# Optimization experiments

Hardware: AMD Instinct MI355X
Metric: run time of the kernel (lower is better)

## Reference

```python
import jax, jax.numpy as jnp
import numpy as np

N = 50000   # total nodes across batched graphs
E = 800000  # total edges
F = 30      # input node features
G = 256     # number of graphs in the disjoint batch
CH = [128, 64, 32]
N_LABELS = 2


def setup_inputs() -> dict:
    key = jax.random.key(0)
    ks = jax.random.split(key, 16)
    x = jax.random.normal(ks[0], (N, F), dtype=jnp.float32)
    edge_weight = jax.random.uniform(ks[1], (E,), dtype=jnp.float32)
    edge_row = jax.random.randint(ks[2], (E,), 0, N, dtype=jnp.int32)
    edge_col = jax.random.randint(ks[3], (E,), 0, N, dtype=jnp.int32)
    seg = jnp.sort(jax.random.randint(ks[4], (N,), 0, G, dtype=jnp.int32))
    # GCSConv params: out = A @ (x W1) + x W2 + b, per layer
    dims = [F] + CH
    params = {}
    kk = 5
    for l in range(3):
        fin, fout = dims[l], dims[l + 1]
        s = 1.0 / np.sqrt(fin)
        params[f"w1_{l+1}"] = jax.random.uniform(ks[kk], (fin, fout), minval=-s, maxval=s, dtype=jnp.float32); kk += 1
        params[f"w2_{l+1}"] = jax.random.uniform(ks[kk], (fin, fout), minval=-s, maxval=s, dtype=jnp.float32); kk += 1
        params[f"b_{l+1}"] = jnp.zeros((fout,), dtype=jnp.float32)
    sd = 1.0 / np.sqrt(CH[-1])
    params["wd"] = jax.random.uniform(ks[kk], (CH[-1], N_LABELS), minval=-sd, maxval=sd, dtype=jnp.float32)
    params["bd"] = jnp.zeros((N_LABELS,), dtype=jnp.float32)
    return {"x": x, "edge_weight": edge_weight, "edge_row": edge_row,
            "edge_col": edge_col, "seg": seg, **params}


def _gcs_conv(x, ew, er, ec, w1, w2, b):
    # spektral GCSConv: relu(A @ (x W1) + x W2 + b) with sparse A in COO form
    h = x @ w1                                   # [N, Fout]
    msgs = ew[:, None] * h[ec]                   # gather along edges [E, Fout]
    agg = jax.ops.segment_sum(msgs, er, num_segments=N)  # SpMM scatter [N, Fout]
    return jax.nn.relu(agg + x @ w2 + b)


def reference(x, edge_weight, edge_row, edge_col, seg,
              w1_1, w2_1, b_1, w1_2, w2_2, b_2, w1_3, w2_3, b_3, wd, bd):
    h = _gcs_conv(x, edge_weight, edge_row, edge_col, w1_1, w2_1, b_1)
    h = _gcs_conv(h, edge_weight, edge_row, edge_col, w1_2, w2_2, b_2)
    h = _gcs_conv(h, edge_weight, edge_row, edge_col, w1_3, w2_3, b_3)
    # GlobalAvgPool: segment mean over graph ids
    sums = jax.ops.segment_sum(h, seg, num_segments=G)               # [G, 32]
    cnts = jax.ops.segment_sum(jnp.ones((N,), h.dtype), seg, num_segments=G)
    pooled = sums / jnp.maximum(cnts, 1.0)[:, None]
    return jax.nn.softmax(pooled @ wd + bd, axis=-1)                 # [G, 2]
```

## Files before the change

### kernel.cpp

```cpp
#include <hip/hip_runtime.h>
#include <hip/hip_fp16.h>

#define N_NODES 50000
#define N_EDGES 800000
#define N_GRAPHS 256
#define NCB 196
#define CHUNK 3125
#define MBLK 782

typedef _Float16 f16x8 __attribute__((ext_vector_type(8)));
typedef float    f32x4 __attribute__((ext_vector_type(4)));

__global__ __launch_bounds__(256)
void hist_prep(const int* __restrict__ ER, const float* __restrict__ X,
               const int* __restrict__ SEG,
               const float* __restrict__ W1, const float* __restrict__ W2,
               const float* __restrict__ W12, const float* __restrict__ W22,
               const float* __restrict__ W13, const float* __restrict__ W23,
               int* __restrict__ ghist, __half* __restrict__ XPh,
               int* __restrict__ start,
               __half* __restrict__ W1f, __half* __restrict__ W2f,
               __half* __restrict__ W3f, float* __restrict__ PS)
{
    int b = blockIdx.x;
    int t = threadIdx.x;
    if (b < 256) {
        __shared__ int h[NCB];
        for (int i = t; i < NCB; i += 256) h[i] = 0;
        __syncthreads();
        int lo = b * CHUNK, hi = lo + CHUNK;
        for (int e = lo + t; e < hi; e += 256) atomicAdd(&h[ER[e] >> 8], 1);
        __syncthreads();
        for (int i = t; i < NCB; i += 256) ghist[i * 256 + b] = h[i];
        return;
    }
    int bid = b - 256;
    if (bid < 6250) {
        int idx = bid * 256 + t;
        int n = idx >> 5;
        int c = idx & 31;
        float v = (c < 30) ? X[n * 30 + c] : 0.f;
        XPh[(size_t)n * 32 + c] = __float2half(v);
    } else if (bid < 6446) {
        int n = (bid - 6250) * 256 + t;
        if (n >= N_NODES) return;
        int g = SEG[n];
        int gprev = (n == 0) ? -1 : SEG[n - 1];
        for (int gg = gprev + 1; gg <= g; ++gg) start[gg] = n;
        if (n == N_NODES - 1)
            for (int gg = g + 1; gg <= N_GRAPHS; ++gg) start[gg] = N_NODES;
    } else if (bid < 6558) {
        int idx = (bid - 6446) * 256 + t;
        if (idx < 8192) {
            int i = idx & 7, c = (idx >> 3) & 15, g = (idx >> 7) & 3;
            int s = (idx >> 9) & 1, n = idx >> 10;
            int k = s * 32 + g * 8 + i, col = n * 16 + c;
            float w = 0.f;
            if (k < 30) w = W1[k * 128 + col];
            else if (k >= 32 && k < 62) w = W2[(k - 32) * 128 + col];
            W1f[idx] = __float2half(w);
        } else if (idx < 24576) {
            int o = idx - 8192;
            int i = o & 7, c = (o >> 3) & 15, g = (o >> 7) & 3;
            int s = (o >> 9) & 3, n = o >> 11;
            int k = s * 32 + g * 8 + i, col = n * 16 + c;
            float w = (col < 64) ? W12[k * 64 + col] : W22[k * 64 + col - 64];
            W2f[o] = __float2half(w);
        } else {
            int o = idx - 24576;
            int i = o & 7, c = (o >> 3) & 15, g = (o >> 7) & 3;
            int s = (o >> 9) & 1, n = o >> 10;
            int k = s * 32 + g * 8 + i, col = n * 16 + c;
            float w = (col < 32) ? W13[k * 32 + col] : W23[k * 32 + col - 32];
            W3f[o] = __float2half(w);
        }
    } else {
        int idx = (bid - 6558) * 256 + t;
        PS[idx] = 0.f;
    }
}

__global__ __launch_bounds__(256)
void scan1(int* __restrict__ ghist, int* __restrict__ bsum)
{
    __shared__ int s[256];
    int t = threadIdx.x, b = blockIdx.x;
    int i = b * 256 + t;
    int v = ghist[i];
    s[t] = v;
    __syncthreads();
    for (int off = 1; off < 256; off <<= 1) {
        int u = (t >= off) ? s[t - off] : 0;
        __syncthreads();
        s[t] += u;
        __syncthreads();
    }
    ghist[i] = s[t] - v;
    if (t == 255) bsum[b] = s[255];
}

__global__ __launch_bounds__(256)
void c_scatter(const int* __restrict__ ER, const int* __restrict__ EC,
               const float* __restrict__ EW, const int* __restrict__ ghist,
               const int* __restrict__ bsum, unsigned int* __restrict__ tmp_sd,
               __half* __restrict__ tmp_w)
{
    __shared__ int s[256];
    __shared__ int cur[NCB];
    int t = threadIdx.x, blk = blockIdx.x;
    int v = (t < NCB) ? bsum[t] : 0;
    s[t] = v;
    __syncthreads();
    for (int off = 1; off < 256; off <<= 1) {
        int u = (t >= off) ? s[t - off] : 0;
        __syncthreads();
        s[t] += u;
        __syncthreads();
    }
    if (t < NCB) cur[t] = (s[t] - v) + ghist[t * 256 + blk];
    __syncthreads();
    int lo = blk * CHUNK, hi = lo + CHUNK;
    for (int e = lo + t; e < hi; e += 256) {
        int d = ER[e];
        int pos = atomicAdd(&cur[d >> 8], 1);
        tmp_sd[pos] = (unsigned int)EC[e] | ((unsigned int)(d & 255) << 16);
        tmp_w[pos] = __float2half(EW[e]);
    }
}

__device__ __forceinline__ void fma8h(float4& a0, float4& a1, float w,
                                      const uint4& raw)
{
    const __half2* hp = (const __half2*)&raw;
    float2 f0 = __half22float2(hp[0]);
    float2 f1 = __half22float2(hp[1]);
    float2 f2 = __half22float2(hp[2]);
    float2 f3 = __half22float2(hp[3]);
    a0.x = fmaf(w, f0.x, a0.x); a0.y = fmaf(w, f0.y, a0.y);
    a0.z = fmaf(w, f1.x, a0.z); a0.w = fmaf(w, f1.y, a0.w);
    a1.x = fmaf(w, f2.x, a1.x); a1.y = fmaf(w, f2.y, a1.y);
    a1.z = fmaf(w, f3.x, a1.z); a1.w = fmaf(w, f3.y, a1.w);
}

__device__ __forceinline__ unsigned int relu2(unsigned int u)
{
    unsigned int lo = (u & 0x8000u)     ? 0u : (u & 0x0000FFFFu);
    unsigned int hi = (u & 0x80000000u) ? 0u : (u & 0xFFFF0000u);
    return lo | hi;
}

__global__ __launch_bounds__(512)
void bsort_aggx(const unsigned int* __restrict__ tmp_sd, const __half* __restrict__ tmp_w,
                const int* __restrict__ bsum, const __half* __restrict__ XPh,
                unsigned int* __restrict__ packed, int* __restrict__ rowptr,
                __half* __restrict__ CIa)
{
    __shared__ int s[256];
    __shared__ int hist[256];
    __shared__ int cur[256];
    __shared__ int r0arr[257];
    int t = threadIdx.x, b = blockIdx.x;

    if (t < 256) s[t] = (t < NCB) ? bsum[t] : 0;
    __syncthreads();
    for (int off = 1; off < 256; off <<= 1) {
        int u = 0;
        if (t < 256 && t >= off) u = s[t - off];
        __syncthreads();
        if (t < 256) s[t] += u;
        __syncthreads();
    }
    int cntb = bsum[b];
    int base = s[b] - cntb;
    int end  = base + cntb;
    __syncthreads();

    if (t < 256) hist[t] = 0;
    __syncthreads();
    for (int j = base + t; j < end; j += 512)
        atomicAdd(&hist[(tmp_sd[j] >> 16) & 255], 1);
    __syncthreads();
    int hv = 0;
    if (t < 256) { hv = hist[t]; s[t] = hv; }
    __syncthreads();
    for (int off = 1; off < 256; off <<= 1) {
        int u = 0;
        if (t < 256 && t >= off) u = s[t - off];
        __syncthreads();
        if (t < 256) s[t] += u;
        __syncthreads();
    }
    if (t < 256) {
        int excl = s[t] - hv;
        int n = b * 256 + t;
        if (n < N_NODES) rowptr[n] = base + excl;
        if (b == NCB - 1 && t == 0) rowptr[N_NODES] = N_EDGES;
        r0arr[t] = base + excl;
        cur[t] = base + excl;
        if (t == 0) r0arr[256] = end;
    }
    __syncthreads();
    for (int j = base + t; j < end; j += 512) {
        unsigned int sd = tmp_sd[j];
        unsigned short hb = __half_as_ushort(tmp_w[j]);
        int pos = atomicAdd(&cur[(sd >> 16) & 255], 1);
        packed[pos] = (sd & 0xFFFF) | ((unsigned int)hb << 16);
    }
    __syncthreads();

    #pragma unroll
    for (int pass = 0; pass < 2; ++pass) {
        int local = pass * 128 + (t >> 2);
        int q = t & 3;
        int n = b * 256 + local;
        if (n < N_NODES) {
            int r0 = r0arr[local], r1 = r0arr[local + 1];
            float4 acc0 = make_float4(0.f, 0.f, 0.f, 0.f);
            float4 acc1 = make_float4(0.f, 0.f, 0.f, 0.f);
            int j = r0;
            for (; j + 3 < r1; j += 4) {
                unsigned int ra = packed[j],     rb = packed[j + 1];
                unsigned int rc = packed[j + 2], rd = packed[j + 3];
                uint4 rawa = *(const uint4*)(XPh + (size_t)(ra & 0xFFFF) * 32 + q * 8);
                uint4 rawb = *(const uint4*)(XPh + (size_t)(rb & 0xFFFF) * 32 + q * 8);
                uint4 rawc = *(const uint4*)(XPh + (size_t)(rc & 0xFFFF) * 32 + q * 8);
                uint4 rawd = *(const uint4*)(XPh + (size_t)(rd & 0xFFFF) * 32 + q * 8);
                float wa = __half2float(__ushort_as_half((unsigned short)(ra >> 16)));
                float wb = __half2float(__ushort_as_half((unsigned short)(rb >> 16)));
                float wc = __half2float(__ushort_as_half((unsigned short)(rc >> 16)));
                float wd = __half2float(__ushort_as_half((unsigned short)(rd >> 16)));
                fma8h(acc0, acc1, wa, rawa);
                fma8h(acc0, acc1, wb, rawb);
                fma8h(acc0, acc1, wc, rawc);
                fma8h(acc0, acc1, wd, rawd);
            }
            for (; j < r1; ++j) {
                unsigned int r = packed[j];
                uint4 raw = *(const uint4*)(XPh + (size_t)(r & 0xFFFF) * 32 + q * 8);
                float w = __half2float(__ushort_as_half((unsigned short)(r >> 16)));
                fma8h(acc0, acc1, w, raw);
            }
            __half2 hb2[4];
            hb2[0] = __float22half2_rn(make_float2(acc0.x, acc0.y));
            hb2[1] = __float22half2_rn(make_float2(acc0.z, acc0.w));
            hb2[2] = __float22half2_rn(make_float2(acc1.x, acc1.y));
            hb2[3] = __float22half2_rn(make_float2(acc1.z, acc1.w));
            *(uint4*)(CIa + (size_t)n * 32 + q * 8) = *(uint4*)&hb2[0];
        }
    }
}

__global__ __launch_bounds__(256)
void dense12_mfma(const __half* __restrict__ CIa, const __half* __restrict__ XPh,
                  const __half* __restrict__ W1f, const float* __restrict__ B1,
                  const __half* __restrict__ W2f, const float* __restrict__ B2,
                  __half* __restrict__ H2a, __half* __restrict__ H2b,
                  __half* __restrict__ A2a, __half* __restrict__ A2b)
{
    __shared__ __align__(16) __half As[64 * 72];
    __shared__ __align__(16) __half Hs[64 * 136];
    const int tid = threadIdx.x;
    const int m0 = blockIdx.x * 64;
    const int lane = tid & 63;
    const int w  = tid >> 6;
    const int lr = lane & 15;
    const int lg = lane >> 4;

    for (int idx = tid; idx < 512; idx += 256) {
        int row = idx >> 3, c8 = idx & 7;
        int gm = m0 + row;
        uint4 v = make_uint4(0, 0, 0, 0);
        if (gm < N_NODES) {
            const __half* src = (c8 < 4) ? (CIa + (size_t)gm * 32 + c8 * 8)
                                         : (XPh + (size_t)gm * 32 + (c8 - 4) * 8);
            v = *(const uint4*)src;
        }
        *(uint4*)(As + row * 72 + c8 * 8) = v;
    }
    __syncthreads();

    f32x4 acc[4][2];
    #pragma unroll
    for (int m = 0; m < 4; ++m)
        #pragma unroll
        for (int j = 0; j < 2; ++j)
            acc[m][j] = (f32x4){0.f, 0.f, 0.f, 0.f};

    #pragma unroll
    for (int s = 0; s < 2; ++s) {
        f16x8 a[4];
        #pragma unroll
        for (int m = 0; m < 4; ++m)
            a[m] = *(const f16x8*)(As + (m * 16 + lr) * 72 + s * 32 + lg * 8);
        #pragma unroll
        for (int j = 0; j < 2; ++j) {
            const int n = 2 * w + j;
            f16x8 b = *(const f16x8*)(W1f + (((n * 2 + s) * 4 + lg) * 16 + lr) * 8);
            #pragma unroll
            for (int m = 0; m < 4; ++m)
                acc[m][j] = __builtin_amdgcn_mfma_f32_16x16x32_f16(a[m], b, acc[m][j], 0, 0, 0);
        }
    }

    #pragma unroll
    for (int j = 0; j < 2; ++j) {
        const int n = 2 * w + j;
        const float bias = B1[n * 16 + lr];
        #pragma unroll
        for (int m = 0; m < 4; ++m)
            #pragma unroll
            for (int r = 0; r < 4; ++r) {
                float v = fmaxf(acc[m][j][r] + bias, 0.f);
                Hs[(m * 16 + lg * 4 + r) * 136 + n * 16 + lr] = __float2half(v);
            }
    }
    __syncthreads();

    f32x4 acc2[4][2];
    #pragma unroll
    for (int m = 0; m < 4; ++m)
        #pragma unroll
        for (int j = 0; j < 2; ++j)
            acc2[m][j] = (f32x4){0.f, 0.f, 0.f, 0.f};

    #pragma unroll
    for (int s = 0; s < 4; ++s) {
        f16x8 a[4];
        #pragma unroll
        for (int m = 0; m < 4; ++m)
            a[m] = *(const f16x8*)(Hs + (m * 16 + lr) * 136 + s * 32 + lg * 8);
        #pragma unroll
        for (int j = 0; j < 2; ++j) {
            const int n = 2 * w + j;
            f16x8 b = *(const f16x8*)(W2f + (((n * 4 + s) * 4 + lg) * 16 + lr) * 8);
            #pragma unroll
            for (int m = 0; m < 4; ++m)
                acc2[m][j] = __builtin_amdgcn_mfma_f32_16x16x32_f16(a[m], b, acc2[m][j], 0, 0, 0);
        }
    }
    __syncthreads();

    #pragma unroll
    for (int j = 0; j < 2; ++j) {
        const int n = 2 * w + j;
        const float bias = (n >= 4) ? B2[(n - 4) * 16 + lr] : 0.f;
        #pragma unroll
        for (int m = 0; m < 4; ++m)
            #pragma unroll
            for (int r = 0; r < 4; ++r)
                Hs[(m * 16 + lg * 4 + r) * 136 + n * 16 + lr] =
                    __float2half(acc2[m][j][r] + bias);
    }
    __syncthreads();

    for (int idx = tid; idx < 1024; idx += 256) {
        int row = idx >> 4, c8 = idx & 15;
        int gm = m0 + row;
        if (gm < N_NODES) {
            uint4 v = *(const uint4*)(Hs + row * 136 + c8 * 8);
            __half* dst;
            switch (c8 >> 2) {
            case 0:  dst = H2a; break;
            case 1:  dst = H2b; break;
            case 2:  dst = A2a; break;
            default: dst = A2b; break;
            }
            *(uint4*)(dst + (size_t)gm * 32 + (c8 & 3) * 8) = v;
        }
    }
}

__global__ __launch_bounds__(256)
void dense3_mfma(const __half* __restrict__ A2a, const __half* __restrict__ A2b,
                 const __half* __restrict__ W3f,
                 const float* __restrict__ B3, __half* __restrict__ H3h,
                 __half* __restrict__ B2h)
{
    __shared__ __align__(16) __half As[64 * 72];
    __shared__ __align__(16) __half Os[64 * 72];
    const int tid = threadIdx.x;
    const int m0 = blockIdx.x * 64;
    const int lane = tid & 63;
    const int w  = tid >> 6;
    const int lr = lane & 15;
    const int lg = lane >> 4;

    for (int idx = tid; idx < 512; idx += 256) {
        int row = idx >> 3, c8 = idx & 7;
        int gm = m0 + row;
        uint4 v = make_uint4(0, 0, 0, 0);
        if (gm < N_NODES) {
            const __half* src = (c8 < 4) ? (A2a + (size_t)gm * 32 + c8 * 8)
                                         : (A2b + (size_t)gm * 32 + (c8 - 4) * 8);
            v = *(const uint4*)src;
        }
        v.x = relu2(v.x); v.y = relu2(v.y); v.z = relu2(v.z); v.w = relu2(v.w);
        *(uint4*)(As + row * 72 + c8 * 8) = v;
    }
    __syncthreads();

    f32x4 acc[4];
    #pragma unroll
    for (int m = 0; m < 4; ++m) acc[m] = (f32x4){0.f, 0.f, 0.f, 0.f};

    #pragma unroll
    for (int s = 0; s < 2; ++s) {
        f16x8 b = *(const f16x8*)(W3f + (((w * 2 + s) * 4 + lg) * 16 + lr) * 8);
        #pragma unroll
        for (int m = 0; m < 4; ++m) {
            f16x8 a = *(const f16x8*)(As + (m * 16 + lr) * 72 + s * 32 + lg * 8);
            acc[m] = __builtin_amdgcn_mfma_f32_16x16x32_f16(a, b, acc[m], 0, 0, 0);
        }
    }

    const float bias = (w >= 2) ? B3[(w - 2) * 16 + lr] : 0.f;
    #pragma unroll
    for (int m = 0; m < 4; ++m)
        #pragma unroll
        for (int r = 0; r < 4; ++r)
            Os[(m * 16 + lg * 4 + r) * 72 + w * 16 + lr] =
                __float2half(acc[m][r] + bias);
    __syncthreads();

    for (int idx = tid; idx < 512; idx += 256) {
        int row = idx >> 3, c8 = idx & 7;
        int gm = m0 + row;
        if (gm < N_NODES) {
            uint4 v = *(const uint4*)(Os + row * 72 + c8 * 8);
            if (c8 < 4) *(uint4*)(H3h + (size_t)gm * 32 + c8 * 8) = v;
            else        *(uint4*)(B2h + (size_t)gm * 32 + (c8 - 4) * 8) = v;
        }
    }
}

template<int FOUT>
__global__ __launch_bounds__(256)
void spmm_h(const __half* __restrict__ H, const int* __restrict__ rowptr,
            const unsigned int* __restrict__ packed, __half* __restrict__ AGGh)
{
    constexpr int T = FOUT / 8;
    int tid = threadIdx.x;
    int local = tid / T;
    int q = tid % T;
    int n = blockIdx.x * (256 / T) + local;
    if (n >= N_NODES) return;
    int r0 = rowptr[n], r1 = rowptr[n + 1];
    __half* ap = AGGh + (size_t)n * FOUT + q * 8;
    float4 acc0, acc1;
    {
        uint4 raw = *(const uint4*)ap;
        const __half2* hp = (const __half2*)&raw;
        float2 f0 = __half22float2(hp[0]);
        float2 f1 = __half22float2(hp[1]);
        float2 f2 = __half22float2(hp[2]);
        float2 f3 = __half22float2(hp[3]);
        acc0 = make_float4(f0.x, f0.y, f1.x, f1.y);
        acc1 = make_float4(f2.x, f2.y, f3.x, f3.y);
    }
    int j = r0;
    for (; j + 3 < r1; j += 4) {
        unsigned int ra = packed[j],     rb = packed[j + 1];
        unsigned int rc = packed[j + 2], rd = packed[j + 3];
        uint4 rawa = *(const uint4*)(H + (size_t)(ra & 0xFFFF) * FOUT + q * 8);
        uint4 rawb = *(const uint4*)(H + (size_t)(rb & 0xFFFF) * FOUT + q * 8);
        uint4 rawc = *(const uint4*)(H + (size_t)(rc & 0xFFFF) * FOUT + q * 8);
        uint4 rawd = *(const uint4*)(H + (size_t)(rd & 0xFFFF) * FOUT + q * 8);
        float wa = __half2float(__ushort_as_half((unsigned short)(ra >> 16)));
        float wb = __half2float(__ushort_as_half((unsigned short)(rb >> 16)));
        float wc = __half2float(__ushort_as_half((unsigned short)(rc >> 16)));
        float wd = __half2float(__ushort_as_half((unsigned short)(rd >> 16)));
        fma8h(acc0, acc1, wa, rawa);
        fma8h(acc0, acc1, wb, rawb);
        fma8h(acc0, acc1, wc, rawc);
        fma8h(acc0, acc1, wd, rawd);
    }
    for (; j < r1; ++j) {
        unsigned int r = packed[j];
        uint4 raw = *(const uint4*)(H + (size_t)(r & 0xFFFF) * FOUT + q * 8);
        float w = __half2float(__ushort_as_half((unsigned short)(r >> 16)));
        fma8h(acc0, acc1, w, raw);
    }
    __half2 hb[4];
    hb[0] = __float22half2_rn(make_float2(acc0.x, acc0.y));
    hb[1] = __float22half2_rn(make_float2(acc0.z, acc0.w));
    hb[2] = __float22half2_rn(make_float2(acc1.x, acc1.y));
    hb[3] = __float22half2_rn(make_float2(acc1.z, acc1.w));
    *(uint4*)ap = *(uint4*)&hb[0];
}

__global__ __launch_bounds__(256)
void spmm_pool(const __half* __restrict__ H, const int* __restrict__ rowptr,
               const unsigned int* __restrict__ packed,
               const __half* __restrict__ Bse, const int* __restrict__ SEG,
               float* __restrict__ PS)
{
    __shared__ float ps[65][32];
    int tid = threadIdx.x;
    int local = tid >> 2;
    int q = tid & 3;
    int n0 = blockIdx.x * 64;
    int n = n0 + local;
    for (int i = tid; i < 65 * 32; i += 256) ((float*)ps)[i] = 0.f;
    __syncthreads();
    int g0 = SEG[n0];
    if (n < N_NODES) {
        int g = SEG[n];
        int r0 = rowptr[n], r1 = rowptr[n + 1];
        float4 acc0, acc1;
        {
            uint4 raw = *(const uint4*)(Bse + (size_t)n * 32 + q * 8);
            const __half2* hp = (const __half2*)&raw;
            float2 f0 = __half22float2(hp[0]);
            float2 f1 = __half22float2(hp[1]);
            float2 f2 = __half22float2(hp[2]);
            float2 f3 = __half22float2(hp[3]);
            acc0 = make_float4(f0.x, f0.y, f1.x, f1.y);
            acc1 = make_float4(f2.x, f2.y, f3.x, f3.y);
        }
        int j = r0;
        for (; j + 3 < r1; j += 4) {
            unsigned int ra = packed[j],     rb = packed[j + 1];
            unsigned int rc = packed[j + 2], rd = packed[j + 3];
            uint4 rawa = *(const uint4*)(H + (size_t)(ra & 0xFFFF) * 32 + q * 8);
            uint4 rawb = *(const uint4*)(H + (size_t)(rb & 0xFFFF) * 32 + q * 8);
            uint4 rawc = *(const uint4*)(H + (size_t)(rc & 0xFFFF) * 32 + q * 8);
            uint4 rawd = *(const uint4*)(H + (size_t)(rd & 0xFFFF) * 32 + q * 8);
            float wa = __half2float(__ushort_as_half((unsigned short)(ra >> 16)));
            float wb = __half2float(__ushort_as_half((unsigned short)(rb >> 16)));
            float wc = __half2float(__ushort_as_half((unsigned short)(rc >> 16)));
            float wd = __half2float(__ushort_as_half((unsigned short)(rd >> 16)));
            fma8h(acc0, acc1, wa, rawa);
            fma8h(acc0, acc1, wb, rawb);
            fma8h(acc0, acc1, wc, rawc);
            fma8h(acc0, acc1, wd, rawd);
        }
        for (; j < r1; ++j) {
            unsigned int r = packed[j];
            uint4 raw = *(const uint4*)(H + (size_t)(r & 0xFFFF) * 32 + q * 8);
            float w = __half2float(__ushort_as_half((unsigned short)(r >> 16)));
            fma8h(acc0, acc1, w, raw);
        }
        float* dst = &ps[g - g0][q * 8];
        atomicAdd(&dst[0], fmaxf(acc0.x, 0.f));
        atomicAdd(&dst[1], fmaxf(acc0.y, 0.f));
        atomicAdd(&dst[2], fmaxf(acc0.z, 0.f));
        atomicAdd(&dst[3], fmaxf(acc0.w, 0.f));
        atomicAdd(&dst[4], fmaxf(acc1.x, 0.f));
        atomicAdd(&dst[5], fmaxf(acc1.y, 0.f));
        atomicAdd(&dst[6], fmaxf(acc1.z, 0.f));
        atomicAdd(&dst[7], fmaxf(acc1.w, 0.f));
    }
    __syncthreads();
    int nlast = n0 + 63;
    if (nlast >= N_NODES) nlast = N_NODES - 1;
    int span = SEG[nlast] - g0 + 1;
    for (int i = tid; i < span * 32; i += 256) {
        float v = ps[i >> 5][i & 31];
        if (v != 0.f)
            atomicAdd(&PS[(size_t)(g0 + (i >> 5)) * 32 + (i & 31)], v);
    }
}

__global__ __launch_bounds__(256)
void head_kernel(const float* __restrict__ PS, const int* __restrict__ start,
                 const float* __restrict__ WD, const float* __restrict__ BD,
                 float* __restrict__ OUT)
{
    int g = threadIdx.x;
    int s = start[g], e = start[g + 1];
    float inv = (e > s) ? 1.0f / (float)(e - s) : 1.0f;
    float l0 = 0.f, l1 = 0.f;
    #pragma unroll
    for (int j = 0; j < 32; ++j) {
        float p = PS[g * 32 + j] * inv;
        l0 = fmaf(p, WD[j * 2 + 0], l0);
        l1 = fmaf(p, WD[j * 2 + 1], l1);
    }
    l0 += BD[0]; l1 += BD[1];
    float m = fmaxf(l0, l1);
    float e0 = expf(l0 - m), e1 = expf(l1 - m);
    float si = 1.0f / (e0 + e1);
    OUT[g * 2 + 0] = e0 * si;
    OUT[g * 2 + 1] = e1 * si;
}

extern "C" void kernel_launch(void* const* d_in, const int* in_sizes, int n_in,
                              void* d_out, int out_size, void* d_ws, size_t ws_size,
                              hipStream_t stream)
{
    const float* x    = (const float*)d_in[0];
    const float* ew   = (const float*)d_in[1];
    const int*   er   = (const int*)d_in[2];
    const int*   ec   = (const int*)d_in[3];
    const int*   seg  = (const int*)d_in[4];
    const float* w1_1 = (const float*)d_in[5];
    const float* w2_1 = (const float*)d_in[6];
    const float* b_1  = (const float*)d_in[7];
    const float* w1_2 = (const float*)d_in[8];
    const float* w2_2 = (const float*)d_in[9];
    const float* b_2  = (const float*)d_in[10];
    const float* w1_3 = (const float*)d_in[11];
    const float* w2_3 = (const float*)d_in[12];
    const float* b_3  = (const float*)d_in[13];
    const float* wd   = (const float*)d_in[14];
    const float* bd   = (const float*)d_in[15];

    float* ws = (float*)d_ws;
    int*   IW = (int*)d_ws;
    __half* XPh    = (__half*)ws;
    __half* CIa    = (__half*)(ws + 800000);
    unsigned int* tmp_sd = (unsigned int*)(ws + 1600000);
    __half* tmp_w  = (__half*)(ws + 2400000);
    __half* H2a    = (__half*)(ws + 3200000);
    __half* H2b    = (__half*)(ws + 4000000);
    __half* A2a    = (__half*)(ws + 4800000);
    __half* A2b    = (__half*)(ws + 5600000);
    __half* H3h    = (__half*)(ws + 6400000);
    __half* B2h    = (__half*)(ws + 7200000);
    unsigned int* packed = (unsigned int*)(IW + 8000000);
    int*    rowptr = IW + 9000000;
    int*    ghist  = IW + 9060000;
    int*    bsum   = IW + 9115000;
    int*    start  = IW + 9120000;
    __half* W1f    = (__half*)(ws + 9125000);
    __half* W2f    = (__half*)(ws + 9130000);
    __half* W3f    = (__half*)(ws + 9139000);
    float*  PS     = ws + 9145000;

    dim3 blk(256);

    hist_prep<<<dim3(256 + 6590), blk, 0, stream>>>(er, x, seg, w1_1, w2_1,
                                                    w1_2, w2_2, w1_3, w2_3,
                                                    ghist, XPh, start,
                                                    W1f, W2f, W3f, PS);
    scan1<<<dim3(NCB), blk, 0, stream>>>(ghist, bsum);
    c_scatter<<<dim3(256), blk, 0, stream>>>(er, ec, ew, ghist, bsum, tmp_sd, tmp_w);
    bsort_aggx<<<dim3(NCB), dim3(512), 0, stream>>>(tmp_sd, tmp_w, bsum, XPh,
                                                    packed, rowptr, CIa);

    dense12_mfma<<<dim3(MBLK), blk, 0, stream>>>(CIa, XPh, W1f, b_1,
                                                 W2f, b_2, H2a, H2b, A2a, A2b);
    spmm_h<32><<<dim3(MBLK), blk, 0, stream>>>(H2a, rowptr, packed, A2a);
    spmm_h<32><<<dim3(MBLK), blk, 0, stream>>>(H2b, rowptr, packed, A2b);
    dense3_mfma<<<dim3(MBLK), blk, 0, stream>>>(A2a, A2b, w1_3 ? W3f : W3f, b_3, H3h, B2h);
    spmm_pool<<<dim3(MBLK), blk, 0, stream>>>(H3h, rowptr, packed, B2h, seg, PS);
    head_kernel<<<dim3(1), blk, 0, stream>>>(PS, start, wd, bd, (float*)d_out);
}
```

Baseline: 190.5 us.

## Fuse layer-2 SpMM into layer-3 dense MFMA kernel with 64-wide rows

Merges the two 32-column spmm_h passes and dense3_mfma into one kernel, spmm_dense3. It gathers 64-wide half rows of H2, adds the self term, applies ReLU and writes straight into shared memory, where the MFMA product for layer 3 reads it. H2 and A2 are now stored as contiguous 64-column rows, so each edge gather is a single 128-byte row read instead of two separate 64-byte passes. This removes two kernel launches and the global-memory round trip of the layer-2 aggregate. In exchange it uses 512-thread blocks, and the irregular gather now sits in the same kernel as the MFMA phase.

```diff
diff --git a/kernel.cpp b/kernel.cpp
--- a/kernel.cpp
+++ b/kernel.cpp
@@ -142,13 +142,6 @@
     a1.z = fmaf(w, f3.x, a1.z); a1.w = fmaf(w, f3.y, a1.w);
 }
 
-__device__ __forceinline__ unsigned int relu2(unsigned int u)
-{
-    unsigned int lo = (u & 0x8000u)     ? 0u : (u & 0x0000FFFFu);
-    unsigned int hi = (u & 0x80000000u) ? 0u : (u & 0xFFFF0000u);
-    return lo | hi;
-}
-
 __global__ __launch_bounds__(512)
 void bsort_aggx(const unsigned int* __restrict__ tmp_sd, const __half* __restrict__ tmp_w,
                 const int* __restrict__ bsum, const __half* __restrict__ XPh,
@@ -254,8 +247,7 @@
 void dense12_mfma(const __half* __restrict__ CIa, const __half* __restrict__ XPh,
                   const __half* __restrict__ W1f, const float* __restrict__ B1,
                   const __half* __restrict__ W2f, const float* __restrict__ B2,
-                  __half* __restrict__ H2a, __half* __restrict__ H2b,
-                  __half* __restrict__ A2a, __half* __restrict__ A2b)
+                  __half* __restrict__ H2h, __half* __restrict__ A2h)
 {
     __shared__ __align__(16) __half As[64 * 72];
     __shared__ __align__(16) __half Hs[64 * 136];
@@ -358,21 +350,16 @@
         int gm = m0 + row;
         if (gm < N_NODES) {
             uint4 v = *(const uint4*)(Hs + row * 136 + c8 * 8);
-            __half* dst;
-            switch (c8 >> 2) {
-            case 0:  dst = H2a; break;
-            case 1:  dst = H2b; break;
-            case 2:  dst = A2a; break;
-            default: dst = A2b; break;
-            }
-            *(uint4*)(dst + (size_t)gm * 32 + (c8 & 3) * 8) = v;
-        }
-    }
-}
-
-__global__ __launch_bounds__(256)
-void dense3_mfma(const __half* __restrict__ A2a, const __half* __restrict__ A2b,
-                 const __half* __restrict__ W3f,
+            if (c8 < 8) *(uint4*)(H2h + (size_t)gm * 64 + c8 * 8) = v;
+            else        *(uint4*)(A2h + (size_t)gm * 64 + (c8 - 8) * 8) = v;
+        }
+    }
+}
+
+__global__ __launch_bounds__(512)
+void spmm_dense3(const __half* __restrict__ H2h, const int* __restrict__ rowptr,
+                 const unsigned int* __restrict__ packed,
+                 const __half* __restrict__ A2h, const __half* __restrict__ W3f,
                  const float* __restrict__ B3, __half* __restrict__ H3h,
                  __half* __restrict__ B2h)
 {
@@ -380,50 +367,93 @@
     __shared__ __align__(16) __half Os[64 * 72];
     const int tid = threadIdx.x;
     const int m0 = blockIdx.x * 64;
+
+    {
+        int local = tid >> 3;
+        int q = tid & 7;
+        int n = m0 + local;
+        float4 acc0 = make_float4(0.f, 0.f, 0.f, 0.f);
+        float4 acc1 = make_float4(0.f, 0.f, 0.f, 0.f);
+        if (n < N_NODES) {
+            {
+                uint4 raw = *(const uint4*)(A2h + (size_t)n * 64 + q * 8);
+                const __half2* hp = (const __half2*)&raw;
+                float2 f0 = __half22float2(hp[0]);
+                float2 f1 = __half22float2(hp[1]);
+                float2 f2 = __half22float2(hp[2]);
+                float2 f3 = __half22float2(hp[3]);
+                acc0 = make_float4(f0.x, f0.y, f1.x, f1.y);
+                acc1 = make_float4(f2.x, f2.y, f3.x, f3.y);
+            }
+            int r0 = rowptr[n], r1 = rowptr[n + 1];
+            int j = r0;
+            for (; j + 3 < r1; j += 4) {
+                unsigned int ra = packed[j],     rb = packed[j + 1];
+                unsigned int rc = packed[j + 2], rd = packed[j + 3];
+                uint4 rawa = *(const uint4*)(H2h + (size_t)(ra & 0xFFFF) * 64 + q * 8);
+                uint4 rawb = *(const uint4*)(H2h + (size_t)(rb & 0xFFFF) * 64 + q * 8);
+                uint4 rawc = *(const uint4*)(H2h + (size_t)(rc & 0xFFFF) * 64 + q * 8);
+                uint4 rawd = *(const uint4*)(H2h + (size_t)(rd & 0xFFFF) * 64 + q * 8);
+                float wa = __half2float(__ushort_as_half((unsigned short)(ra >> 16)));
+                float wb = __half2float(__ushort_as_half((unsigned short)(rb >> 16)));
+                float wc = __half2float(__ushort_as_half((unsigned short)(rc >> 16)));
+                float wd = __half2float(__ushort_as_half((unsigned short)(rd >> 16)));
+                fma8h(acc0, acc1, wa, rawa);
+                fma8h(acc0, acc1, wb, rawb);
+                fma8h(acc0, acc1, wc, rawc);
+                fma8h(acc0, acc1, wd, rawd);
+            }
+            for (; j < r1; ++j) {
+                unsigned int r = packed[j];
+                uint4 raw = *(const uint4*)(H2h + (size_t)(r & 0xFFFF) * 64 + q * 8);
+                float w = __half2float(__ushort_as_half((unsigned short)(r >> 16)));
+                fma8h(acc0, acc1, w, raw);
+            }
+        }
+        __half2 hb[4];
+        hb[0] = __float22half2_rn(make_float2(fmaxf(acc0.x, 0.f), fmaxf(acc0.y, 0.f)));
+        hb[1] = __float22half2_rn(make_float2(fmaxf(acc0.z, 0.f), fmaxf(acc0.w, 0.f)));
+        hb[2] = __float22half2_rn(make_float2(fmaxf(acc1.x, 0.f), fmaxf(acc1.y, 0.f)));
+        hb[3] = __float22half2_rn(make_float2(fmaxf(acc1.z, 0.f), fmaxf(acc1.w, 0.f)));
+        *(uint4*)(As + local * 72 + q * 8) = *(uint4*)&hb[0];
+    }
+    __syncthreads();
+
     const int lane = tid & 63;
     const int w  = tid >> 6;
+    const int wm = w >> 2;
+    const int wn = w & 3;
     const int lr = lane & 15;
     const int lg = lane >> 4;
 
-    for (int idx = tid; idx < 512; idx += 256) {
-        int row = idx >> 3, c8 = idx & 7;
-        int gm = m0 + row;
-        uint4 v = make_uint4(0, 0, 0, 0);
-        if (gm < N_NODES) {
-            const __half* src = (c8 < 4) ? (A2a + (size_t)gm * 32 + c8 * 8)
-                                         : (A2b + (size_t)gm * 32 + (c8 - 4) * 8);
-            v = *(const uint4*)src;
-        }
-        v.x = relu2(v.x); v.y = relu2(v.y); v.z = relu2(v.z); v.w = relu2(v.w);
-        *(uint4*)(As + row * 72 + c8 * 8) = v;
-    }
-    __syncthreads();
-
-    f32x4 acc[4];
-    #pragma unroll
-    for (int m = 0; m < 4; ++m) acc[m] = (f32x4){0.f, 0.f, 0.f, 0.f};
+    f32x4 acc[2];
+    acc[0] = (f32x4){0.f, 0.f, 0.f, 0.f};
+    acc[1] = (f32x4){0.f, 0.f, 0.f, 0.f};
 
     #pragma unroll
     for (int s = 0; s < 2; ++s) {
-        f16x8 b = *(const f16x8*)(W3f + (((w * 2 + s) * 4 + lg) * 16 + lr) * 8);
-        #pragma unroll
-        for (int m = 0; m < 4; ++m) {
-            f16x8 a = *(const f16x8*)(As + (m * 16 + lr) * 72 + s * 32 + lg * 8);
+        f16x8 b = *(const f16x8*)(W3f + (((wn * 2 + s) * 4 + lg) * 16 + lr) * 8);
+        #pragma unroll
+        for (int m = 0; m < 2; ++m) {
+            int mm = wm * 2 + m;
+            f16x8 a = *(const f16x8*)(As + (mm * 16 + lr) * 72 + s * 32 + lg * 8);
             acc[m] = __builtin_amdgcn_mfma_f32_16x16x32_f16(a, b, acc[m], 0, 0, 0);
         }
     }
 
-    const float bias = (w >= 2) ? B3[(w - 2) * 16 + lr] : 0.f;
-    #pragma unroll
-    for (int m = 0; m < 4; ++m)
+    const float bias = (wn >= 2) ? B3[(wn - 2) * 16 + lr] : 0.f;
+    #pragma unroll
+    for (int m = 0; m < 2; ++m) {
+        int mm = wm * 2 + m;
         #pragma unroll
         for (int r = 0; r < 4; ++r)
-            Os[(m * 16 + lg * 4 + r) * 72 + w * 16 + lr] =
+            Os[(mm * 16 + lg * 4 + r) * 72 + wn * 16 + lr] =
                 __float2half(acc[m][r] + bias);
-    __syncthreads();
-
-    for (int idx = tid; idx < 512; idx += 256) {
-        int row = idx >> 3, c8 = idx & 7;
+    }
+    __syncthreads();
+
+    {
+        int row = tid >> 3, c8 = tid & 7;
         int gm = m0 + row;
         if (gm < N_NODES) {
             uint4 v = *(const uint4*)(Os + row * 72 + c8 * 8);
@@ -431,61 +461,6 @@
             else        *(uint4*)(B2h + (size_t)gm * 32 + (c8 - 4) * 8) = v;
         }
     }
-}
-
-template<int FOUT>
-__global__ __launch_bounds__(256)
-void spmm_h(const __half* __restrict__ H, const int* __restrict__ rowptr,
-            const unsigned int* __restrict__ packed, __half* __restrict__ AGGh)
-{
-    constexpr int T = FOUT / 8;
-    int tid = threadIdx.x;
-    int local = tid / T;
-    int q = tid % T;
-    int n = blockIdx.x * (256 / T) + local;
-    if (n >= N_NODES) return;
-    int r0 = rowptr[n], r1 = rowptr[n + 1];
-    __half* ap = AGGh + (size_t)n * FOUT + q * 8;
-    float4 acc0, acc1;
-    {
-        uint4 raw = *(const uint4*)ap;
-        const __half2* hp = (const __half2*)&raw;
-        float2 f0 = __half22float2(hp[0]);
-        float2 f1 = __half22float2(hp[1]);
-        float2 f2 = __half22float2(hp[2]);
-        float2 f3 = __half22float2(hp[3]);
-        acc0 = make_float4(f0.x, f0.y, f1.x, f1.y);
-        acc1 = make_float4(f2.x, f2.y, f3.x, f3.y);
-    }
-    int j = r0;
-    for (; j + 3 < r1; j += 4) {
-        unsigned int ra = packed[j],     rb = packed[j + 1];
-        unsigned int rc = packed[j + 2], rd = packed[j + 3];
-        uint4 rawa = *(const uint4*)(H + (size_t)(ra & 0xFFFF) * FOUT + q * 8);
-        uint4 rawb = *(const uint4*)(H + (size_t)(rb & 0xFFFF) * FOUT + q * 8);
-        uint4 rawc = *(const uint4*)(H + (size_t)(rc & 0xFFFF) * FOUT + q * 8);
-        uint4 rawd = *(const uint4*)(H + (size_t)(rd & 0xFFFF) * FOUT + q * 8);
-        float wa = __half2float(__ushort_as_half((unsigned short)(ra >> 16)));
-        float wb = __half2float(__ushort_as_half((unsigned short)(rb >> 16)));
-        float wc = __half2float(__ushort_as_half((unsigned short)(rc >> 16)));
-        float wd = __half2float(__ushort_as_half((unsigned short)(rd >> 16)));
-        fma8h(acc0, acc1, wa, rawa);
-        fma8h(acc0, acc1, wb, rawb);
-        fma8h(acc0, acc1, wc, rawc);
-        fma8h(acc0, acc1, wd, rawd);
-    }
-    for (; j < r1; ++j) {
-        unsigned int r = packed[j];
-        uint4 raw = *(const uint4*)(H + (size_t)(r & 0xFFFF) * FOUT + q * 8);
-        float w = __half2float(__ushort_as_half((unsigned short)(r >> 16)));
-        fma8h(acc0, acc1, w, raw);
-    }
-    __half2 hb[4];
-    hb[0] = __float22half2_rn(make_float2(acc0.x, acc0.y));
-    hb[1] = __float22half2_rn(make_float2(acc0.z, acc0.w));
-    hb[2] = __float22half2_rn(make_float2(acc1.x, acc1.y));
-    hb[3] = __float22half2_rn(make_float2(acc1.z, acc1.w));
-    *(uint4*)ap = *(uint4*)&hb[0];
 }
 
 __global__ __launch_bounds__(256)
@@ -611,10 +586,8 @@
     __half* CIa    = (__half*)(ws + 800000);
     unsigned int* tmp_sd = (unsigned int*)(ws + 1600000);
     __half* tmp_w  = (__half*)(ws + 2400000);
-    __half* H2a    = (__half*)(ws + 3200000);
-    __half* H2b    = (__half*)(ws + 4000000);
-    __half* A2a    = (__half*)(ws + 4800000);
-    __half* A2b    = (__half*)(ws + 5600000);
+    __half* H2h    = (__half*)(ws + 3200000);
+    __half* A2h    = (__half*)(ws + 4800000);
     __half* H3h    = (__half*)(ws + 6400000);
     __half* B2h    = (__half*)(ws + 7200000);
     unsigned int* packed = (unsigned int*)(IW + 8000000);
@@ -639,10 +612,9 @@
                                                     packed, rowptr, CIa);
 
     dense12_mfma<<<dim3(MBLK), blk, 0, stream>>>(CIa, XPh, W1f, b_1,
-                                                 W2f, b_2, H2a, H2b, A2a, A2b);
-    spmm_h<32><<<dim3(MBLK), blk, 0, stream>>>(H2a, rowptr, packed, A2a);
-    spmm_h<32><<<dim3(MBLK), blk, 0, stream>>>(H2b, rowptr, packed, A2b);
-    dense3_mfma<<<dim3(MBLK), blk, 0, stream>>>(A2a, A2b, w1_3 ? W3f : W3f, b_3, H3h, B2h);
+                                                 W2f, b_2, H2h, A2h);
+    spmm_dense3<<<dim3(MBLK), dim3(512), 0, stream>>>(H2h, rowptr, packed, A2h,
+                                                      W3f, b_3, H3h, B2h);
     spmm_pool<<<dim3(MBLK), blk, 0, stream>>>(H3h, rowptr, packed, B2h, seg, PS);
     head_kernel<<<dim3(1), blk, 0, stream>>>(PS, start, wd, bd, (float*)d_out);
 }
```

After: 182.4 us. 4.3% less time.
